# Kernel tuning notes

Measured on AMD Instinct MI355X. Metric: run time of the kernel, lower is better.

Reference implementation:

```python
import jax, jax.numpy as jnp
import numpy as np

B, T, S, R, D, F = 256, 8, 200, 8, 64, 20


def setup_inputs() -> dict:
    key = jax.random.key(0)
    ks = jax.random.split(key, 8)
    # 0.1 scale keeps attention logits in a reasonable range (like trained embeddings)
    seq = 0.1 * jax.random.normal(ks[0], (B, S, D), dtype=jnp.float32)
    delta_t_n = jax.random.uniform(ks[1], (B, S), dtype=jnp.float32)  # normalized time gaps
    target = 0.1 * jax.random.normal(ks[2], (B, T, D), dtype=jnp.float32)
    target_value = 0.1 * jax.random.normal(ks[3], (B, T, R, D), dtype=jnp.float32)
    valid_mask = jax.random.randint(ks[4], (B, 1, S, 1), 0, 2, dtype=jnp.int32)
    rel_emb = 0.1 * jax.random.normal(ks[5], (R, D), dtype=jnp.float32)
    freq_real = 0.1 * jax.random.normal(ks[6], (R, F), dtype=jnp.float32)
    freq_imag = 0.1 * jax.random.normal(ks[7], (R, F), dtype=jnp.float32)
    return dict(seq=seq, delta_t_n=delta_t_n, target=target, target_value=target_value,
                valid_mask=valid_mask, rel_emb=rel_emb, freq_real=freq_real, freq_imag=freq_imag)


def _idft_decay(delta_t_n, freq_real, freq_imag):
    # freqs: concat(linspace(0,1,F)/2, -linspace(0,1,F)/2) -> [2F]
    f = jnp.linspace(0.0, 1.0, F, dtype=jnp.float32) / 2.0
    freqs = jnp.concatenate([f, -f])
    x_real = jnp.concatenate([freq_real, freq_real], axis=-1)   # [R,2F]
    x_imag = jnp.concatenate([freq_imag, -freq_imag], axis=-1)  # [R,2F]
    w = 2.0 * jnp.pi * freqs * delta_t_n[..., None]             # [B,S,2F]
    # [B,S,1,2F] * [1,1,R,2F] -> mean over 2F -> [B,S,R]
    decay = (jnp.cos(w)[:, :, None, :] * x_real[None, None]
             - jnp.sin(w)[:, :, None, :] * x_imag[None, None]).mean(axis=-1) / 2.0
    return decay


def reference(seq, delta_t_n, target, target_value, valid_mask, rel_emb, freq_real, freq_imag):
    # include_val=True branch
    rv = rel_emb[None, None] + target_value              # [B,T,R,D]
    ri = rv * target[:, :, None, :]                      # [B,T,R,D]
    # scores: contraction over D, no [B,T,S,R,D] materialization
    att = jnp.einsum('bsd,btrd->btsr', seq, ri)          # [B,T,S,R]
    att = att - att.max()
    att = jnp.where(valid_mask == 0, -jnp.inf, att)
    att = jax.nn.softmax(att, axis=-2)                   # softmax over seq (S)
    decay = jnp.clip(_idft_decay(delta_t_n, freq_real, freq_imag), 0.0, 1.0)[:, None]  # [B,1,S,R]
    decay = jnp.where(valid_mask == 0, 0.0, decay)
    att = att * decay
    context = jnp.einsum('bsd,btsr->btrd', seq, att)     # [B,T,R,D]
    return context
```

## Files before the change

### kernel.cpp

```cpp
#include <hip/hip_runtime.h>
#include <math.h>

constexpr int kB = 256, kT = 8, kS = 200, kR = 8, kD = 64, kF = 20;
constexpr float kW1 = 3.14159265358979323846f / 19.0f;

typedef __attribute__((ext_vector_type(8))) short s16x8;
typedef __attribute__((ext_vector_type(4))) float f32x4;

union F8 { s16x8 v; unsigned short u[8]; };

__device__ __forceinline__ unsigned short bf_hi(float x, float& hf) {
    unsigned u = __float_as_uint(x) & 0xffff0000u;
    hf = __uint_as_float(u);
    return (unsigned short)(u >> 16);
}
__device__ __forceinline__ unsigned short bf_rne(float x) {
    unsigned v = __float_as_uint(x);
    return (unsigned short)((v + 0x7fffu + ((v >> 16) & 1u)) >> 16);
}

__global__ __launch_bounds__(256) void decay_kernel(
    const float* __restrict__ dt, const float* __restrict__ fr,
    const float* __restrict__ fi, const int* __restrict__ vm,
    float* __restrict__ dec)
{
    const int b = blockIdx.x;
    const int tid = threadIdx.x;
    const int r = tid >> 5, j = tid & 31;

    float frr[kF], fir[kF];
    {
        const float4* f4 = (const float4*)(fr + r * kF);
        const float4* g4 = (const float4*)(fi + r * kF);
#pragma unroll
        for (int c = 0; c < 5; ++c) {
            float4 a = f4[c], g = g4[c];
            frr[4*c+0]=a.x; frr[4*c+1]=a.y; frr[4*c+2]=a.z; frr[4*c+3]=a.w;
            fir[4*c+0]=g.x; fir[4*c+1]=g.y; fir[4*c+2]=g.z; fir[4*c+3]=g.w;
        }
    }
#pragma unroll
    for (int it = 0; it < 7; ++it) {
        const int s = j + 32 * it;
        if (s < kS) {
            const float tt = dt[b * kS + s];
            const bool valid = vm[b * kS + s] != 0;
            float s1, c1;
            __sincosf(kW1 * tt, &s1, &c1);
            float ck = c1, sk = s1;
            float acc = frr[0] + c1 * frr[1] - s1 * fir[1];
#pragma unroll
            for (int k = 2; k < kF; ++k) {
                float cn = ck * c1 - sk * s1;
                float sn = sk * c1 + ck * s1;
                ck = cn; sk = sn;
                acc += ck * frr[k] - sk * fir[k];
            }
            float v = fminf(fmaxf(acc * (1.0f / (2.0f * kF)), 0.f), 1.f);
            dec[(b * kR + r) * kS + s] = valid ? v : 0.f;
        }
    }
}

__global__ __launch_bounds__(256) void rda_mfma(
    const float* __restrict__ seq,
    const float* __restrict__ target,
    const float* __restrict__ tv,
    const int*   __restrict__ vm,
    const float* __restrict__ rel,
    const float* __restrict__ dec,
    float* __restrict__ out)
{
    __shared__ unsigned short riBh[16][72], riBl[16][72];
    __shared__ float attr[16][212];
    __shared__ unsigned short ath[16][232], atl[16][232];

    const int o = blockIdx.x, b = o & 255, g = o >> 8, t0 = 2 * g;
    const int tid = threadIdx.x, w = tid >> 6, l = tid & 63;
    const int lm = l & 15, lq = l >> 4;

    {
        const int n = tid >> 4, d0 = (tid & 15) * 4;
        const int tl = n >> 3, r = n & 7;
        const int btl = b * kT + t0 + tl;
        float4 rv  = *(const float4*)(rel + r * kD + d0);
        float4 tvv = *(const float4*)(tv + ((size_t)btl * kR + r) * kD + d0);
        float4 tg  = *(const float4*)(target + (size_t)btl * kD + d0);
        float x[4] = {(rv.x+tvv.x)*tg.x, (rv.y+tvv.y)*tg.y,
                      (rv.z+tvv.z)*tg.z, (rv.w+tvv.w)*tg.w};
        ushort4 h, lo; float hf;
        h.x = bf_hi(x[0], hf); lo.x = bf_rne(x[0] - hf);
        h.y = bf_hi(x[1], hf); lo.y = bf_rne(x[1] - hf);
        h.z = bf_hi(x[2], hf); lo.z = bf_rne(x[2] - hf);
        h.w = bf_hi(x[3], hf); lo.w = bf_rne(x[3] - hf);
        *(ushort4*)&riBh[n][d0] = h;
        *(ushort4*)&riBl[n][d0] = lo;
    }
    __syncthreads();

    for (int Mt = w; Mt < 13; Mt += 4) {
        const int srow = min(Mt * 16 + lm, kS - 1);
        const float* sp = seq + ((size_t)b * kS + srow) * kD;
        F8 ah[2], al[2];
#pragma unroll
        for (int Kt = 0; Kt < 2; ++Kt) {
            const int d0 = Kt * 32 + lq * 8;
            float4 x0 = *(const float4*)(sp + d0);
            float4 x1 = *(const float4*)(sp + d0 + 4);
            float xs[8] = {x0.x,x0.y,x0.z,x0.w,x1.x,x1.y,x1.z,x1.w};
#pragma unroll
            for (int i = 0; i < 8; ++i) {
                float hf; ah[Kt].u[i] = bf_hi(xs[i], hf);
                al[Kt].u[i] = bf_rne(xs[i] - hf);
            }
        }
        f32x4 acc = {0.f, 0.f, 0.f, 0.f};
#pragma unroll
        for (int Kt = 0; Kt < 2; ++Kt) {
            F8 bh, bl;
            bh.v = *(const s16x8*)&riBh[lm][Kt * 32 + lq * 8];
            bl.v = *(const s16x8*)&riBl[lm][Kt * 32 + lq * 8];
            acc = __builtin_amdgcn_mfma_f32_16x16x32_bf16(ah[Kt].v, bh.v, acc, 0, 0, 0);
            acc = __builtin_amdgcn_mfma_f32_16x16x32_bf16(ah[Kt].v, bl.v, acc, 0, 0, 0);
            acc = __builtin_amdgcn_mfma_f32_16x16x32_bf16(al[Kt].v, bh.v, acc, 0, 0, 0);
        }
        *(f32x4*)&attr[lm][Mt * 16 + lq * 4] = acc;
    }
    __syncthreads();

    {
        bool ok0 = vm[b * kS + l] != 0;
        bool ok1 = vm[b * kS + l + 64] != 0;
        bool ok2 = vm[b * kS + l + 128] != 0;
        bool ok3 = (l < 8) && (vm[b * kS + 192 + l] != 0);
        const int s3 = (l < 8) ? 192 + l : kS - 1;
#pragma unroll
        for (int j = 0; j < 4; ++j) {
            const int n = 4 * w + j, r = n & 7;
            float a0 = ok0 ? attr[n][l]       : -INFINITY;
            float a1 = ok1 ? attr[n][l + 64]  : -INFINITY;
            float a2 = ok2 ? attr[n][l + 128] : -INFINITY;
            float a3 = ok3 ? attr[n][s3]      : -INFINITY;
            float m = fmaxf(fmaxf(a0, a1), fmaxf(a2, a3));
#pragma unroll
            for (int off = 32; off; off >>= 1) m = fmaxf(m, __shfl_xor(m, off));
            float e0 = __expf(a0 - m), e1 = __expf(a1 - m);
            float e2 = __expf(a2 - m), e3 = ok3 ? __expf(a3 - m) : 0.f;
            float ssum = e0 + e1 + e2 + e3;
#pragma unroll
            for (int off = 32; off; off >>= 1) ssum += __shfl_xor(ssum, off);
            const float inv = 1.0f / ssum;
            const float* dg = dec + ((size_t)b * kR + r) * kS;
            float p0 = e0 * inv * dg[l];
            float p1 = e1 * inv * dg[l + 64];
            float p2 = e2 * inv * dg[l + 128];
            float p3 = ok3 ? e3 * inv * dg[192 + l] : 0.f;
            float hf;
            ath[n][l]       = bf_hi(p0, hf); atl[n][l]       = bf_rne(p0 - hf);
            ath[n][l + 64]  = bf_hi(p1, hf); atl[n][l + 64]  = bf_rne(p1 - hf);
            ath[n][l + 128] = bf_hi(p2, hf); atl[n][l + 128] = bf_rne(p2 - hf);
            if (l < 32) {
                float pv = (l < 8) ? p3 : 0.f;
                ath[n][192 + l] = bf_hi(pv, hf); atl[n][192 + l] = bf_rne(pv - hf);
            }
        }
    }
    __syncthreads();

    {
        const int dcol = w * 16 + lm;
        f32x4 acc = {0.f, 0.f, 0.f, 0.f};
        for (int Kt = 0; Kt < 7; ++Kt) {
            F8 bh, bl;
#pragma unroll
            for (int i = 0; i < 8; ++i) {
                const int s = Kt * 32 + lq * 8 + i;
                float x = (s < kS) ? seq[((size_t)b * kS + s) * kD + dcol] : 0.f;
                float hf; bh.u[i] = bf_hi(x, hf); bl.u[i] = bf_rne(x - hf);
            }
            F8 ahh, alo;
            ahh.v = *(const s16x8*)&ath[lm][Kt * 32 + lq * 8];
            alo.v = *(const s16x8*)&atl[lm][Kt * 32 + lq * 8];
            acc = __builtin_amdgcn_mfma_f32_16x16x32_bf16(ahh.v, bh.v, acc, 0, 0, 0);
            acc = __builtin_amdgcn_mfma_f32_16x16x32_bf16(ahh.v, bl.v, acc, 0, 0, 0);
            acc = __builtin_amdgcn_mfma_f32_16x16x32_bf16(alo.v, bh.v, acc, 0, 0, 0);
        }
#pragma unroll
        for (int i = 0; i < 4; ++i) {
            const int n = lq * 4 + i, tl = n >> 3, r = n & 7;
            out[(((size_t)(b * kT + t0 + tl)) * kR + r) * kD + dcol] = acc[i];
        }
    }
}

extern "C" void kernel_launch(void* const* d_in, const int* in_sizes, int n_in,
                              void* d_out, int out_size, void* d_ws, size_t ws_size,
                              hipStream_t stream) {
    const float* seq    = (const float*)d_in[0];
    const float* dt     = (const float*)d_in[1];
    const float* target = (const float*)d_in[2];
    const float* tv     = (const float*)d_in[3];
    const int*   vm     = (const int*)  d_in[4];
    const float* rel    = (const float*)d_in[5];
    const float* fr     = (const float*)d_in[6];
    const float* fi     = (const float*)d_in[7];
    float* out = (float*)d_out;
    float* dec = (float*)d_ws;

    decay_kernel<<<kB, 256, 0, stream>>>(dt, fr, fi, vm, dec);
    rda_mfma<<<kB * 4, 256, 0, stream>>>(seq, target, tv, vm, rel, dec, out);
}
```

Measured before the change: 92.37 us.

## Precompute bf16 hi/lo splits of seq, plus a transposed copy, in a prep kernel

The decay kernel becomes a prep kernel that also splits seq once into bf16 hi/lo arrays and writes a zero-padded transposed copy through shared memory. The main kernel then loads ready-made bf16 fragments with vector loads. Before, each of the four t-group blocks per batch reconverted seq, and the second GEMM did strided scalar global loads. The cost is extra global writes and reads of about twice the seq footprint in bf16, plus workspace use.

```diff
diff --git a/kernel.cpp b/kernel.cpp
--- a/kernel.cpp
+++ b/kernel.cpp
@@ -2,12 +2,11 @@
 #include <math.h>
 
 constexpr int kB = 256, kT = 8, kS = 200, kR = 8, kD = 64, kF = 20;
+constexpr int kSP = 224;
 constexpr float kW1 = 3.14159265358979323846f / 19.0f;
 
 typedef __attribute__((ext_vector_type(8))) short s16x8;
 typedef __attribute__((ext_vector_type(4))) float f32x4;
-
-union F8 { s16x8 v; unsigned short u[8]; };
 
 __device__ __forceinline__ unsigned short bf_hi(float x, float& hf) {
     unsigned u = __float_as_uint(x) & 0xffff0000u;
@@ -19,17 +18,46 @@
     return (unsigned short)((v + 0x7fffu + ((v >> 16) & 1u)) >> 16);
 }
 
-__global__ __launch_bounds__(256) void decay_kernel(
-    const float* __restrict__ dt, const float* __restrict__ fr,
-    const float* __restrict__ fi, const int* __restrict__ vm,
-    float* __restrict__ dec)
+__global__ __launch_bounds__(256) void prep_kernel(
+    const float* __restrict__ seq,
+    const float* __restrict__ dt,
+    const float* __restrict__ fr,
+    const float* __restrict__ fi,
+    const int*   __restrict__ vm,
+    float* __restrict__ dec,
+    unsigned short* __restrict__ seqH,
+    unsigned short* __restrict__ seqL,
+    unsigned short* __restrict__ seqTH,
+    unsigned short* __restrict__ seqTL)
 {
-    const int b = blockIdx.x;
-    const int tid = threadIdx.x;
-    const int r = tid >> 5, j = tid & 31;
-
-    float frr[kF], fir[kF];
-    {
+    __shared__ unsigned short lh[kS][66], ll[kS][66];
+
+    const int b = blockIdx.x, tid = threadIdx.x;
+
+    {
+        const float4* sb = (const float4*)(seq + (size_t)b * kS * kD);
+        unsigned short* gh = seqH + (size_t)b * kS * kD;
+        unsigned short* gl = seqL + (size_t)b * kS * kD;
+        for (int idx = tid; idx < kS * kD / 4; idx += 256) {
+            float4 x = sb[idx];
+            const int s = idx >> 4, d0 = (idx & 15) * 4;
+            ushort4 h, lo; float hf;
+            h.x = bf_hi(x.x, hf); lo.x = bf_rne(x.x - hf);
+            h.y = bf_hi(x.y, hf); lo.y = bf_rne(x.y - hf);
+            h.z = bf_hi(x.z, hf); lo.z = bf_rne(x.z - hf);
+            h.w = bf_hi(x.w, hf); lo.w = bf_rne(x.w - hf);
+            *(ushort4*)&gh[idx * 4] = h;
+            *(ushort4*)&gl[idx * 4] = lo;
+            *(ushort2*)&lh[s][d0]     = make_ushort2(h.x, h.y);
+            *(ushort2*)&lh[s][d0 + 2] = make_ushort2(h.z, h.w);
+            *(ushort2*)&ll[s][d0]     = make_ushort2(lo.x, lo.y);
+            *(ushort2*)&ll[s][d0 + 2] = make_ushort2(lo.z, lo.w);
+        }
+    }
+
+    {
+        const int r = tid >> 5, j = tid & 31;
+        float frr[kF], fir[kF];
         const float4* f4 = (const float4*)(fr + r * kF);
         const float4* g4 = (const float4*)(fi + r * kF);
 #pragma unroll
@@ -38,37 +66,51 @@
             frr[4*c+0]=a.x; frr[4*c+1]=a.y; frr[4*c+2]=a.z; frr[4*c+3]=a.w;
             fir[4*c+0]=g.x; fir[4*c+1]=g.y; fir[4*c+2]=g.z; fir[4*c+3]=g.w;
         }
-    }
-#pragma unroll
-    for (int it = 0; it < 7; ++it) {
-        const int s = j + 32 * it;
-        if (s < kS) {
-            const float tt = dt[b * kS + s];
-            const bool valid = vm[b * kS + s] != 0;
-            float s1, c1;
-            __sincosf(kW1 * tt, &s1, &c1);
-            float ck = c1, sk = s1;
-            float acc = frr[0] + c1 * frr[1] - s1 * fir[1];
-#pragma unroll
-            for (int k = 2; k < kF; ++k) {
-                float cn = ck * c1 - sk * s1;
-                float sn = sk * c1 + ck * s1;
-                ck = cn; sk = sn;
-                acc += ck * frr[k] - sk * fir[k];
+#pragma unroll
+        for (int it = 0; it < 7; ++it) {
+            const int s = j + 32 * it;
+            if (s < kS) {
+                const float tt = dt[b * kS + s];
+                const bool valid = vm[b * kS + s] != 0;
+                float s1, c1;
+                __sincosf(kW1 * tt, &s1, &c1);
+                float ck = c1, sk = s1;
+                float acc = frr[0] + c1 * frr[1] - s1 * fir[1];
+#pragma unroll
+                for (int k = 2; k < kF; ++k) {
+                    float cn = ck * c1 - sk * s1;
+                    float sn = sk * c1 + ck * s1;
+                    ck = cn; sk = sn;
+                    acc += ck * frr[k] - sk * fir[k];
+                }
+                float v = fminf(fmaxf(acc * (1.0f / (2.0f * kF)), 0.f), 1.f);
+                dec[(b * kR + r) * kS + s] = valid ? v : 0.f;
             }
-            float v = fminf(fmaxf(acc * (1.0f / (2.0f * kF)), 0.f), 1.f);
-            dec[(b * kR + r) * kS + s] = valid ? v : 0.f;
+        }
+    }
+    __syncthreads();
+
+    {
+        unsigned short* th = seqTH + (size_t)b * kD * kSP;
+        unsigned short* tl = seqTL + (size_t)b * kD * kSP;
+        for (int idx = tid; idx < kD * kSP; idx += 256) {
+            const int d = idx / kSP, s = idx - d * kSP;
+            th[idx] = (s < kS) ? lh[s][d] : (unsigned short)0;
+            tl[idx] = (s < kS) ? ll[s][d] : (unsigned short)0;
         }
     }
 }
 
 __global__ __launch_bounds__(256) void rda_mfma(
-    const float* __restrict__ seq,
     const float* __restrict__ target,
     const float* __restrict__ tv,
     const int*   __restrict__ vm,
     const float* __restrict__ rel,
     const float* __restrict__ dec,
+    const unsigned short* __restrict__ seqH,
+    const unsigned short* __restrict__ seqL,
+    const unsigned short* __restrict__ seqTH,
+    const unsigned short* __restrict__ seqTL,
     float* __restrict__ out)
 {
     __shared__ unsigned short riBh[16][72], riBl[16][72];
@@ -81,8 +123,8 @@
 
     {
         const int n = tid >> 4, d0 = (tid & 15) * 4;
-        const int tl = n >> 3, r = n & 7;
-        const int btl = b * kT + t0 + tl;
+        const int tl_ = n >> 3, r = n & 7;
+        const int btl = b * kT + t0 + tl_;
         float4 rv  = *(const float4*)(rel + r * kD + d0);
         float4 tvv = *(const float4*)(tv + ((size_t)btl * kR + r) * kD + d0);
         float4 tg  = *(const float4*)(target + (size_t)btl * kD + d0);
@@ -100,29 +142,19 @@
 
     for (int Mt = w; Mt < 13; Mt += 4) {
         const int srow = min(Mt * 16 + lm, kS - 1);
-        const float* sp = seq + ((size_t)b * kS + srow) * kD;
-        F8 ah[2], al[2];
+        const unsigned short* ph = seqH + ((size_t)b * kS + srow) * kD;
+        const unsigned short* pl = seqL + ((size_t)b * kS + srow) * kD;
+        f32x4 acc = {0.f, 0.f, 0.f, 0.f};
 #pragma unroll
         for (int Kt = 0; Kt < 2; ++Kt) {
             const int d0 = Kt * 32 + lq * 8;
-            float4 x0 = *(const float4*)(sp + d0);
-            float4 x1 = *(const float4*)(sp + d0 + 4);
-            float xs[8] = {x0.x,x0.y,x0.z,x0.w,x1.x,x1.y,x1.z,x1.w};
-#pragma unroll
-            for (int i = 0; i < 8; ++i) {
-                float hf; ah[Kt].u[i] = bf_hi(xs[i], hf);
-                al[Kt].u[i] = bf_rne(xs[i] - hf);
-            }
-        }
-        f32x4 acc = {0.f, 0.f, 0.f, 0.f};
-#pragma unroll
-        for (int Kt = 0; Kt < 2; ++Kt) {
-            F8 bh, bl;
-            bh.v = *(const s16x8*)&riBh[lm][Kt * 32 + lq * 8];
-            bl.v = *(const s16x8*)&riBl[lm][Kt * 32 + lq * 8];
-            acc = __builtin_amdgcn_mfma_f32_16x16x32_bf16(ah[Kt].v, bh.v, acc, 0, 0, 0);
-            acc = __builtin_amdgcn_mfma_f32_16x16x32_bf16(ah[Kt].v, bl.v, acc, 0, 0, 0);
-            acc = __builtin_amdgcn_mfma_f32_16x16x32_bf16(al[Kt].v, bh.v, acc, 0, 0, 0);
+            s16x8 ah = *(const s16x8*)&ph[d0];
+            s16x8 al = *(const s16x8*)&pl[d0];
+            s16x8 bh = *(const s16x8*)&riBh[lm][d0];
+            s16x8 bl = *(const s16x8*)&riBl[lm][d0];
+            acc = __builtin_amdgcn_mfma_f32_16x16x32_bf16(ah, bh, acc, 0, 0, 0);
+            acc = __builtin_amdgcn_mfma_f32_16x16x32_bf16(ah, bl, acc, 0, 0, 0);
+            acc = __builtin_amdgcn_mfma_f32_16x16x32_bf16(al, bh, acc, 0, 0, 0);
         }
         *(f32x4*)&attr[lm][Mt * 16 + lq * 4] = acc;
     }
@@ -169,26 +201,24 @@
 
     {
         const int dcol = w * 16 + lm;
+        const unsigned short* th = seqTH + ((size_t)b * kD + dcol) * kSP;
+        const unsigned short* tl_ = seqTL + ((size_t)b * kD + dcol) * kSP;
         f32x4 acc = {0.f, 0.f, 0.f, 0.f};
+#pragma unroll
         for (int Kt = 0; Kt < 7; ++Kt) {
-            F8 bh, bl;
-#pragma unroll
-            for (int i = 0; i < 8; ++i) {
-                const int s = Kt * 32 + lq * 8 + i;
-                float x = (s < kS) ? seq[((size_t)b * kS + s) * kD + dcol] : 0.f;
-                float hf; bh.u[i] = bf_hi(x, hf); bl.u[i] = bf_rne(x - hf);
-            }
-            F8 ahh, alo;
-            ahh.v = *(const s16x8*)&ath[lm][Kt * 32 + lq * 8];
-            alo.v = *(const s16x8*)&atl[lm][Kt * 32 + lq * 8];
-            acc = __builtin_amdgcn_mfma_f32_16x16x32_bf16(ahh.v, bh.v, acc, 0, 0, 0);
-            acc = __builtin_amdgcn_mfma_f32_16x16x32_bf16(ahh.v, bl.v, acc, 0, 0, 0);
-            acc = __builtin_amdgcn_mfma_f32_16x16x32_bf16(alo.v, bh.v, acc, 0, 0, 0);
+            const int s0 = Kt * 32 + lq * 8;
+            s16x8 bh  = *(const s16x8*)&th[s0];
+            s16x8 bl  = *(const s16x8*)&tl_[s0];
+            s16x8 ahh = *(const s16x8*)&ath[lm][s0];
+            s16x8 alo = *(const s16x8*)&atl[lm][s0];
+            acc = __builtin_amdgcn_mfma_f32_16x16x32_bf16(ahh, bh, acc, 0, 0, 0);
+            acc = __builtin_amdgcn_mfma_f32_16x16x32_bf16(ahh, bl, acc, 0, 0, 0);
+            acc = __builtin_amdgcn_mfma_f32_16x16x32_bf16(alo, bh, acc, 0, 0, 0);
         }
 #pragma unroll
         for (int i = 0; i < 4; ++i) {
-            const int n = lq * 4 + i, tl = n >> 3, r = n & 7;
-            out[(((size_t)(b * kT + t0 + tl)) * kR + r) * kD + dcol] = acc[i];
+            const int n = lq * 4 + i, tl2 = n >> 3, r = n & 7;
+            out[(((size_t)(b * kT + t0 + tl2)) * kR + r) * kD + dcol] = acc[i];
         }
     }
 }
@@ -205,8 +235,15 @@
     const float* fr     = (const float*)d_in[6];
     const float* fi     = (const float*)d_in[7];
     float* out = (float*)d_out;
+
     float* dec = (float*)d_ws;
-
-    decay_kernel<<<kB, 256, 0, stream>>>(dt, fr, fi, vm, dec);
-    rda_mfma<<<kB * 4, 256, 0, stream>>>(seq, target, tv, vm, rel, dec, out);
-}
+    unsigned short* seqH  = (unsigned short*)((char*)d_ws + 1638400);
+    unsigned short* seqL  = seqH + (size_t)kB * kS * kD;
+    unsigned short* seqTH = seqL + (size_t)kB * kS * kD;
+    unsigned short* seqTL = seqTH + (size_t)kB * kD * kSP;
+
+    prep_kernel<<<kB, 256, 0, stream>>>(seq, dt, fr, fi, vm,
+                                        dec, seqH, seqL, seqTH, seqTL);
+    rda_mfma<<<kB * 4, 256, 0, stream>>>(target, tv, vm, rel, dec,
+                                         seqH, seqL, seqTH, seqTL, out);
+}
```

Measured after the change: 104.9 us. 13.6% more time.
